# Optimization experiments

Hardware: AMD Instinct MI355X
Metric: run time of the kernel (lower is better)

Reference implementation:

```python
import jax, jax.numpy as jnp
import numpy as np

DEPTH = 64
BATCH = 8388608  # 2**23, ~100 MB per fp32 activation


def setup_inputs() -> dict:
    key = jax.random.key(0)
    kx, kw = jax.random.split(key)
    x = jax.random.normal(kx, (BATCH, 3), dtype=jnp.float32)
    # depth stacked 3x3 weight matrices, matching nn.Linear(3,3,bias=False).weight per layer
    W = jax.random.normal(kw, (DEPTH, 3, 3), dtype=jnp.float32) * (1.0 / np.sqrt(3.0))
    return {"x": x, "W": W}


def reference(x, W):
    # Sequential chain: x <- x @ W_l^T for each layer l (nn.Linear applies x @ W.T)
    def step(h, w):
        return h @ w.T, None

    out, _ = jax.lax.scan(step, x, W)
    return out
```

## Files before the change

kernel.cpp:

```cpp
#include <hip/hip_runtime.h>
#include <hip/hip_bf16.h>


#define DEPTH 64
#define BLOCK 256
#define CHUNK (BLOCK * 3)

__global__ __launch_bounds__(64) void fold_weights(const float* __restrict__ W,
                                                   float* __restrict__ P) {
    __shared__ double M[DEPTH][9];
    const int t = threadIdx.x;
    const float* Wl = W + t * 9;
    #pragma unroll
    for (int k = 0; k < 3; ++k)
        #pragma unroll
        for (int j = 0; j < 3; ++j)
            M[t][k * 3 + j] = (double)Wl[j * 3 + k];
    __syncthreads();
    for (int s = 1; s < DEPTH; s <<= 1) {
        if ((t & (2 * s - 1)) == 0) {
            double a[9], b[9], c[9];
            #pragma unroll
            for (int i = 0; i < 9; ++i) { a[i] = M[t][i]; b[i] = M[t + s][i]; }
            #pragma unroll
            for (int i = 0; i < 3; ++i)
                #pragma unroll
                for (int j = 0; j < 3; ++j)
                    c[i * 3 + j] = a[i * 3 + 0] * b[0 * 3 + j]
                                 + a[i * 3 + 1] * b[1 * 3 + j]
                                 + a[i * 3 + 2] * b[2 * 3 + j];
            #pragma unroll
            for (int i = 0; i < 9; ++i) M[t][i] = c[i];
        }
        __syncthreads();
    }
    if (t < 9) P[t] = (float)M[0][t];
}

__global__ __launch_bounds__(BLOCK) void apply_chain(
        const float4* __restrict__ x4, float4* __restrict__ o4,
        const float* __restrict__ P) {
    __shared__ float4 s4[CHUNK];
    const int tid = threadIdx.x;
    const long long base = (long long)blockIdx.x * CHUNK;

    #pragma unroll
    for (int k = 0; k < 3; ++k)
        s4[k * BLOCK + tid] = x4[base + k * BLOCK + tid];

    const float p00 = P[0], p01 = P[1], p02 = P[2];
    const float p10 = P[3], p11 = P[4], p12 = P[5];
    const float p20 = P[6], p21 = P[7], p22 = P[8];

    __syncthreads();

    float4 a = s4[3 * tid];
    float4 b = s4[3 * tid + 1];
    float4 c = s4[3 * tid + 2];

    float4 oa, ob, oc;
    oa.x = fmaf(a.x, p00, fmaf(a.y, p10, a.z * p20));
    oa.y = fmaf(a.x, p01, fmaf(a.y, p11, a.z * p21));
    oa.z = fmaf(a.x, p02, fmaf(a.y, p12, a.z * p22));
    oa.w = fmaf(a.w, p00, fmaf(b.x, p10, b.y * p20));
    ob.x = fmaf(a.w, p01, fmaf(b.x, p11, b.y * p21));
    ob.y = fmaf(a.w, p02, fmaf(b.x, p12, b.y * p22));
    ob.z = fmaf(b.z, p00, fmaf(b.w, p10, c.x * p20));
    ob.w = fmaf(b.z, p01, fmaf(b.w, p11, c.x * p21));
    oc.x = fmaf(b.z, p02, fmaf(b.w, p12, c.x * p22));
    oc.y = fmaf(c.y, p00, fmaf(c.z, p10, c.w * p20));
    oc.z = fmaf(c.y, p01, fmaf(c.z, p11, c.w * p21));
    oc.w = fmaf(c.y, p02, fmaf(c.z, p12, c.w * p22));

    s4[3 * tid]     = oa;
    s4[3 * tid + 1] = ob;
    s4[3 * tid + 2] = oc;

    __syncthreads();

    #pragma unroll
    for (int k = 0; k < 3; ++k)
        o4[base + k * BLOCK + tid] = s4[k * BLOCK + tid];
}

extern "C" void kernel_launch(void* const* d_in, const int* in_sizes, int n_in,
                              void* d_out, int out_size, void* d_ws, size_t ws_size,
                              hipStream_t stream) {
    const float* x = (const float*)d_in[0];
    const float* W = (const float*)d_in[1];
    float* out = (float*)d_out;
    float* P = (float*)d_ws;

    fold_weights<<<1, 64, 0, stream>>>(W, P);

    const long long n_floats = (long long)in_sizes[0];
    const long long n4 = n_floats / 4;
    const int grid = (int)(n4 / CHUNK);

    apply_chain<<<grid, BLOCK, 0, stream>>>(
        (const float4*)x, (float4*)out, P);
}
```

Baseline: 180.2 us.

## Drop LDS staging, load strided float4 triples directly with 4 groups per thread

```diff
diff --git a/kernel.cpp b/kernel.cpp
--- a/kernel.cpp
+++ b/kernel.cpp
@@ -4,7 +4,9 @@
 
 #define DEPTH 64
 #define BLOCK 256
-#define CHUNK (BLOCK * 3)
+#define GPT 4
+
+typedef float vf4 __attribute__((ext_vector_type(4)));
 
 __global__ __launch_bounds__(64) void fold_weights(const float* __restrict__ W,
                                                    float* __restrict__ P) {
@@ -38,49 +40,47 @@
 }
 
 __global__ __launch_bounds__(BLOCK) void apply_chain(
-        const float4* __restrict__ x4, float4* __restrict__ o4,
-        const float* __restrict__ P) {
-    __shared__ float4 s4[CHUNK];
+        const vf4* __restrict__ x4, vf4* __restrict__ o4,
+        const float* __restrict__ P, int n_groups) {
     const int tid = threadIdx.x;
-    const long long base = (long long)blockIdx.x * CHUNK;
-
-    #pragma unroll
-    for (int k = 0; k < 3; ++k)
-        s4[k * BLOCK + tid] = x4[base + k * BLOCK + tid];
+    const int base = blockIdx.x * (BLOCK * GPT);
 
     const float p00 = P[0], p01 = P[1], p02 = P[2];
     const float p10 = P[3], p11 = P[4], p12 = P[5];
     const float p20 = P[6], p21 = P[7], p22 = P[8];
 
-    __syncthreads();
-
-    float4 a = s4[3 * tid];
-    float4 b = s4[3 * tid + 1];
-    float4 c = s4[3 * tid + 2];
-
-    float4 oa, ob, oc;
-    oa.x = fmaf(a.x, p00, fmaf(a.y, p10, a.z * p20));
-    oa.y = fmaf(a.x, p01, fmaf(a.y, p11, a.z * p21));
-    oa.z = fmaf(a.x, p02, fmaf(a.y, p12, a.z * p22));
-    oa.w = fmaf(a.w, p00, fmaf(b.x, p10, b.y * p20));
-    ob.x = fmaf(a.w, p01, fmaf(b.x, p11, b.y * p21));
-    ob.y = fmaf(a.w, p02, fmaf(b.x, p12, b.y * p22));
-    ob.z = fmaf(b.z, p00, fmaf(b.w, p10, c.x * p20));
-    ob.w = fmaf(b.z, p01, fmaf(b.w, p11, c.x * p21));
-    oc.x = fmaf(b.z, p02, fmaf(b.w, p12, c.x * p22));
-    oc.y = fmaf(c.y, p00, fmaf(c.z, p10, c.w * p20));
-    oc.z = fmaf(c.y, p01, fmaf(c.z, p11, c.w * p21));
-    oc.w = fmaf(c.y, p02, fmaf(c.z, p12, c.w * p22));
-
-    s4[3 * tid]     = oa;
-    s4[3 * tid + 1] = ob;
-    s4[3 * tid + 2] = oc;
-
-    __syncthreads();
+    vf4 A[GPT][3];
+    #pragma unroll
+    for (int k = 0; k < GPT; ++k) {
+        const int g = base + k * BLOCK + tid;
+        const vf4* p = x4 + 3 * g;
+        A[k][0] = p[0];
+        A[k][1] = p[1];
+        A[k][2] = p[2];
+    }
 
     #pragma unroll
-    for (int k = 0; k < 3; ++k)
-        o4[base + k * BLOCK + tid] = s4[k * BLOCK + tid];
+    for (int k = 0; k < GPT; ++k) {
+        const int g = base + k * BLOCK + tid;
+        const vf4 a = A[k][0], b = A[k][1], c = A[k][2];
+        vf4 oa, ob, oc;
+        oa[0] = fmaf(a[0], p00, fmaf(a[1], p10, a[2] * p20));
+        oa[1] = fmaf(a[0], p01, fmaf(a[1], p11, a[2] * p21));
+        oa[2] = fmaf(a[0], p02, fmaf(a[1], p12, a[2] * p22));
+        oa[3] = fmaf(a[3], p00, fmaf(b[0], p10, b[1] * p20));
+        ob[0] = fmaf(a[3], p01, fmaf(b[0], p11, b[1] * p21));
+        ob[1] = fmaf(a[3], p02, fmaf(b[0], p12, b[1] * p22));
+        ob[2] = fmaf(b[2], p00, fmaf(b[3], p10, c[0] * p20));
+        ob[3] = fmaf(b[2], p01, fmaf(b[3], p11, c[0] * p21));
+        oc[0] = fmaf(b[2], p02, fmaf(b[3], p12, c[0] * p22));
+        oc[1] = fmaf(c[1], p00, fmaf(c[2], p10, c[3] * p20));
+        oc[2] = fmaf(c[1], p01, fmaf(c[2], p11, c[3] * p21));
+        oc[3] = fmaf(c[1], p02, fmaf(c[2], p12, c[3] * p22));
+        vf4* q = o4 + 3 * g;
+        __builtin_nontemporal_store(oa, q);
+        __builtin_nontemporal_store(ob, q + 1);
+        __builtin_nontemporal_store(oc, q + 2);
+    }
 }
 
 extern "C" void kernel_launch(void* const* d_in, const int* in_sizes, int n_in,
@@ -94,9 +94,9 @@
     fold_weights<<<1, 64, 0, stream>>>(W, P);
 
     const long long n_floats = (long long)in_sizes[0];
-    const long long n4 = n_floats / 4;
-    const int grid = (int)(n4 / CHUNK);
+    const int n_groups = (int)(n_floats / 12);
+    const int grid = n_groups / (BLOCK * GPT);
 
     apply_chain<<<grid, BLOCK, 0, stream>>>(
-        (const float4*)x, (float4*)out, P);
+        (const vf4*)x, (vf4*)out, P, n_groups);
 }
```

Result: slower. 201.4 us (+11.7%).
